# Kernel tuning notes

Measured on AMD Instinct MI355X. Metric: run time of the kernel, lower is better.

## Reference

```python
import jax, jax.numpy as jnp
import numpy as np


def _round_ste(v):
    # straight-through rounding (typical LinearQuantize autograd STE)
    return v + jax.lax.stop_gradient(jnp.round(v) - v)


def setup_inputs() -> dict:
    key = jax.random.key(0)
    k1, k2, k3 = jax.random.split(key, 3)
    tokens, d_in, d_out = 8192, 2048, 2048
    x = jax.random.uniform(k1, (tokens, d_in), dtype=jnp.float32)  # non-negative acts
    weight = jax.random.normal(k2, (d_out, d_in), dtype=jnp.float32) * 0.02
    bias = jax.random.normal(k3, (d_out,), dtype=jnp.float32) * 0.02
    return {"x": x, "weight": weight, "bias": bias, "weight_bit": 8}


def reference(x, weight, bias, weight_bit):
    n = 2 ** weight_bit
    # stats computed on detached data (x.data/w.data in torch)
    wd = jax.lax.stop_gradient(weight)
    w_min = wd.min(axis=1)                      # [out]
    w_max = wd.max(axis=1)                      # [out]
    x_max = jax.lax.stop_gradient(x).max()
    scale_x = (n - 1) / jnp.clip(x_max, 1e-8)
    # activation quantization: round(scale_x * x - 0)
    q_x = _round_ste(scale_x * x)               # [T, in]
    # per-channel asymmetric weight quant (quantize_int)
    scale_w = (n - 1) / jnp.clip(w_max - w_min, 1e-8)   # [out]
    zp_w = scale_w * w_min                      # [out]
    q_w = _round_ste(scale_w[:, None] * weight - zp_w[:, None])  # [out, in]
    # bias quantized with combined scale, then clamped
    q_b = jnp.clip(_round_ste(bias * scale_w * scale_x), -n - 1, n)  # [out]
    # fake-int GEMM + zero-point correction + rescale
    mult = jnp.einsum('ti,oi->to', q_x, q_w) + q_b      # [T, out]
    res = mult + zp_w * q_x.sum(-1, keepdims=True)
    return res / scale_x / scale_w
```

## Files before the change

kernel.cpp:

```cpp
#include <hip/hip_runtime.h>
#include <stdint.h>

typedef __attribute__((ext_vector_type(4))) int i32x4;
typedef __attribute__((ext_vector_type(4))) float f32x4;

__device__ inline float wave_max(float v){ for(int o=32;o;o>>=1) v=fmaxf(v,__shfl_xor(v,o)); return v; }
__device__ inline float wave_min(float v){ for(int o=32;o;o>>=1) v=fminf(v,__shfl_xor(v,o)); return v; }
__device__ inline int   wave_sum(int v){ for(int o=32;o;o>>=1) v+=__shfl_xor(v,o); return v; }

__device__ inline void gload16(const void* g, void* l){
  __builtin_amdgcn_global_load_lds((const __attribute__((address_space(1))) char*)g,
                                   (__attribute__((address_space(3))) char*)l, 16, 0, 0);
}

__global__ void k_xmax_partial(const float* __restrict__ x, long long n4,
                               float* __restrict__ partials){
  long long i = (long long)blockIdx.x*blockDim.x + threadIdx.x;
  long long stride = (long long)gridDim.x*blockDim.x;
  const float4* x4 = (const float4*)x;
  float m = 0.f;
  for(; i < n4; i += stride){
    float4 v = x4[i];
    m = fmaxf(m, fmaxf(fmaxf(v.x,v.y),fmaxf(v.z,v.w)));
  }
  m = wave_max(m);
  __shared__ float sm[4];
  int lane = threadIdx.x & 63, wid = threadIdx.x >> 6;
  if(lane==0) sm[wid] = m;
  __syncthreads();
  if(threadIdx.x==0)
    partials[blockIdx.x] = fmaxf(fmaxf(sm[0],sm[1]),fmaxf(sm[2],sm[3]));
}

__global__ void k_wstat(const float* __restrict__ w,
                        const int* __restrict__ wbit,
                        float* __restrict__ scale_w, float* __restrict__ zp_w,
                        float* __restrict__ winv,
                        int* __restrict__ cint, char* __restrict__ qw, int din){
  int row = blockIdx.x, tid = threadIdx.x;
  int lane = tid & 63, wid = tid >> 6;
  const float4* wr4 = (const float4*)(w + (long long)row*din);
  float4 a = wr4[tid*2], b = wr4[tid*2+1];
  float v[8] = {a.x,a.y,a.z,a.w,b.x,b.y,b.z,b.w};
  float mn = v[0], mx = v[0];
  for(int j=1;j<8;j++){ mn=fminf(mn,v[j]); mx=fmaxf(mx,v[j]); }
  float wmn = wave_min(mn), wmx = wave_max(mx);
  __shared__ float smn[4], smx[4];
  __shared__ float s_sw, s_zp;
  if(lane==0){ smn[wid]=wmn; smx[wid]=wmx; }
  __syncthreads();
  if(tid==0){
    float fmn = fminf(fminf(smn[0],smn[1]),fminf(smn[2],smn[3]));
    float fmx = fmaxf(fmaxf(smx[0],smx[1]),fmaxf(smx[2],smx[3]));
    int n = 1 << *wbit;
    float nm1 = (float)(n-1);
    float rngc = fmaxf(__fsub_rn(fmx, fmn), 1e-8f);
    float sw = __fdiv_rn(nm1, rngc);
    float zp = __fmul_rn(sw, fmn);
    s_sw = sw; s_zp = zp;
    scale_w[row] = sw; zp_w[row] = zp;
    winv[row] = __fdiv_rn(rngc, nm1);
  }
  __syncthreads();
  float sw = s_sw, zp = s_zp;
  int qsum = 0; uint32_t lo = 0, hi = 0;
  for(int j=0;j<8;j++){
    int q = (int)rintf(__fsub_rn(__fmul_rn(sw, v[j]), zp));
    qsum += q;
    uint32_t u = (uint32_t)((q - 128) & 0xff);
    if(j<4) lo |= u << (8*j); else hi |= u << (8*(j-4));
  }
  uint32_t* qrow = (uint32_t*)(qw + (long long)row*din);
  qrow[tid*2] = lo; qrow[tid*2+1] = hi;
  int wsum = wave_sum(qsum);
  __shared__ int ssum[4];
  if(lane==0) ssum[wid] = wsum;
  __syncthreads();
  if(tid==0){
    int Sb = ssum[0]+ssum[1]+ssum[2]+ssum[3];
    cint[row] = 128*Sb - 128*128*din;
  }
}

__global__ void k_xquant(const float* __restrict__ x, const int* __restrict__ wbit,
                         const float* __restrict__ partials, int nPart,
                         char* __restrict__ qx, int* __restrict__ Sa, int din){
  int row = blockIdx.x, tid = threadIdx.x;
  int lane = tid & 63, wid = tid >> 6;
  float mm = 0.f;
  for(int i=tid;i<nPart;i+=256) mm = fmaxf(mm, partials[i]);
  mm = wave_max(mm);
  __shared__ float sm[4];
  if(lane==0) sm[wid] = mm;
  __syncthreads();
  const float xmax = fmaxf(fmaxf(sm[0],sm[1]),fmaxf(sm[2],sm[3]));
  int n = 1 << *wbit;
  float nm1 = (float)(n-1);
  float sx = __fdiv_rn(nm1, fmaxf(xmax, 1e-8f));
  const float4* xr4 = (const float4*)(x + (long long)row*din);
  float4 a = xr4[tid*2], b = xr4[tid*2+1];
  float v[8] = {a.x,a.y,a.z,a.w,b.x,b.y,b.z,b.w};
  int qsum = 0; uint32_t lo = 0, hi = 0;
  for(int j=0;j<8;j++){
    int q = (int)rintf(__fmul_rn(sx, v[j]));
    qsum += q;
    uint32_t u = (uint32_t)((q - 128) & 0xff);
    if(j<4) lo |= u << (8*j); else hi |= u << (8*(j-4));
  }
  uint32_t* qrow = (uint32_t*)(qx + (long long)row*din);
  qrow[tid*2] = lo; qrow[tid*2+1] = hi;
  int wsum = wave_sum(qsum);
  __shared__ int ssum[4];
  if(lane==0) ssum[wid] = wsum;
  __syncthreads();
  if(tid==0) Sa[row] = ssum[0]+ssum[1]+ssum[2]+ssum[3];
}

__global__ __launch_bounds__(512, 2) void k_gemm(
    const char* __restrict__ qx, const char* __restrict__ qw,
    const int* __restrict__ Sa, const int* __restrict__ cint,
    const float* __restrict__ scale_w, const float* __restrict__ winv,
    const float* __restrict__ zp_w, const float* __restrict__ bias,
    const int* __restrict__ wbit, const float* __restrict__ partials, int nPart,
    float* __restrict__ out, int T, int dout, int din){
  extern __shared__ char lds[];
  const int tid = threadIdx.x, lane = tid & 63, wid = tid >> 6;
  const int wr = wid >> 2, wc = wid & 3;
  const int nt = din / 128;

  const int bid = blockIdx.x;
  const int nTN = dout >> 8, nTM = T >> 8;
  int tileM, tileN;
  if(nTM == 32 && nTN == 8){
    const int rect = bid & 7, loc = bid >> 3;
    tileM = (rect >> 1)*8 + (loc & 7);
    tileN = (rect & 1)*4 + (loc >> 3);
  } else {
    tileN = bid % nTN; tileM = bid / nTN;
  }

  const int i0 = tid, i1 = tid + 512;
  const int r0 = i0 >> 2, r1 = i1 >> 2;
  const int sc0 = ((i0 & 3) ^ ((r0 >> 1) & 3)) * 16;
  const int sc1 = ((i1 & 3) ^ ((r1 >> 1) & 3)) * 16;
  const char* aS0 = qx + ((long long)tileM*256 + r0)*din + sc0;
  const char* aS1 = qx + ((long long)tileM*256 + r1)*din + sc1;
  const char* bS0 = qw + ((long long)tileN*256 + r0)*din + sc0;
  const char* bS1 = qw + ((long long)tileN*256 + r1)*din + sc1;
  const int d0 = i0*16, d1 = i1*16;

  const int physo = (((lane >> 4) ^ ((lane >> 1) & 3)) * 16);
  const int arowL = wr*128 + (lane & 15);
  const int browL = wc*64  + (lane & 15);

  i32x4 acc[8][4] = {};
  i32x4 af[4], bf[4];

#define STAGE_A(KS, KOFF, NB) do{ \
    gload16(aS0 + (KOFF) + (KS)*64, (NB) + (KS)*16384 + d0); \
    gload16(aS1 + (KOFF) + (KS)*64, (NB) + (KS)*16384 + d1); }while(0)
#define STAGE_B(KS, KOFF, NB) do{ \
    gload16(bS0 + (KOFF) + (KS)*64, (NB) + 32768 + (KS)*16384 + d0); \
    gload16(bS1 + (KOFF) + (KS)*64, (NB) + 32768 + (KS)*16384 + d1); }while(0)

  STAGE_A(0, 0, lds); STAGE_B(0, 0, lds);
  STAGE_A(1, 0, lds); STAGE_B(1, 0, lds);
  asm volatile("s_waitcnt vmcnt(4)" ::: "memory");
  __builtin_amdgcn_s_barrier();

  for(int t = 0; t < nt; ++t){
    char* Ab = lds + (t & 1)*65536;
    char* Bb = Ab + 32768;
    char* NB = lds + ((t & 1)^1)*65536;
    const bool ld = (t + 1 < nt);
    const int koff = (t + 1)*128;

#define PH(MH, KS, DO_B, STAGE_STMT, VM_STMT) do{ \
    if(DO_B){ _Pragma("unroll") \
      for(int ni=0;ni<4;++ni) bf[ni] = *(const i32x4*)(Bb + (KS)*16384 + (browL + ni*16)*64 + physo); } \
    _Pragma("unroll") \
    for(int mi=0;mi<4;++mi) af[mi] = *(const i32x4*)(Ab + (KS)*16384 + (arowL + (MH)*64 + mi*16)*64 + physo); \
    STAGE_STMT; \
    __builtin_amdgcn_s_barrier(); \
    __builtin_amdgcn_s_setprio(1); \
    _Pragma("unroll") \
    for(int mi=0;mi<4;++mi){ _Pragma("unroll") \
      for(int ni=0;ni<4;++ni) \
        acc[(MH)*4+mi][ni] = __builtin_amdgcn_mfma_i32_16x16x64_i8(af[mi], bf[ni], acc[(MH)*4+mi][ni], 0,0,0); } \
    __builtin_amdgcn_s_setprio(0); \
    VM_STMT; \
    __builtin_amdgcn_s_barrier(); }while(0)

    PH(0, 0, true,  if(ld) STAGE_A(0, koff, NB), );
    PH(1, 0, false, if(ld) STAGE_B(0, koff, NB),
       if(ld){ asm volatile("s_waitcnt vmcnt(4)" ::: "memory"); }
       else  { asm volatile("s_waitcnt vmcnt(0)" ::: "memory"); });
    PH(0, 1, true,  if(ld) STAGE_A(1, koff, NB), );
    PH(1, 1, false, if(ld) STAGE_B(1, koff, NB),
       if(ld){ asm volatile("s_waitcnt vmcnt(4)" ::: "memory"); });
#undef PH
  }

  __syncthreads();
  {
    float mm = 0.f;
    for(int i = tid; i < nPart; i += 512) mm = fmaxf(mm, partials[i]);
    mm = wave_max(mm);
    if(lane==0) ((float*)lds)[wid] = mm;
  }
  __syncthreads();
  float xmax = 0.f;
  #pragma unroll
  for(int i=0;i<8;i++) xmax = fmaxf(xmax, ((float*)lds)[i]);

  const int n = 1 << *wbit;
  const float nm1 = (float)(n-1);
  const float xmaxc = fmaxf(xmax, 1e-8f);
  const float sx = __fdiv_rn(nm1, xmaxc);
  const float inv_sx = __fdiv_rn(xmaxc, nm1);
  const int colL = tileN*256 + wc*64 + (lane & 15);
  const int rowL = tileM*256 + wr*128 + ((lane >> 4) * 4);
  float invc[4], zp4[4]; int ci4[4];
  #pragma unroll
  for(int ni=0; ni<4; ++ni){
    int o = colL + ni*16;
    float sw = scale_w[o];
    float qbf = rintf(__fmul_rn(__fmul_rn(bias[o], sw), sx));
    qbf = fminf(fmaxf(qbf, -(float)(n+1)), (float)n);
    ci4[ni] = cint[o] + (int)qbf;
    invc[ni] = __fmul_rn(winv[o], inv_sx);
    zp4[ni]  = zp_w[o];
  }

  float* ebuf = (float*)lds;
  const int lwr  = wr*16 + ((lane >> 4) * 4);
  const int lcol = wc*64 + (lane & 15);
  #pragma unroll
  for(int mi=0; mi<8; ++mi){
    int rb = rowL + mi*16;
    int sav[4];
    #pragma unroll
    for(int r=0; r<4; ++r) sav[r] = Sa[rb + r];
    __syncthreads();
    #pragma unroll
    for(int ni=0; ni<4; ++ni){
      #pragma unroll
      for(int r=0; r<4; ++r){
        int iv = acc[mi][ni][r] + 128*sav[r] + ci4[ni];
        float f = (float)iv + zp4[ni]*(float)sav[r];
        int row = lwr + r, col = lcol + ni*16;
        ebuf[row*256 + (col ^ (((row>>2)&3)<<4))] = __fmul_rn(f, invc[ni]);
      }
    }
    __syncthreads();
    #pragma unroll
    for(int p=0; p<4; ++p){
      int idx = tid + p*512;
      int lr = idx >> 6, cc = (idx & 63)*4;
      f32x4 v = *(const f32x4*)&ebuf[lr*256 + (cc ^ (((lr>>2)&3)<<4))];
      int gr = tileM*256 + (lr>>4)*128 + mi*16 + (lr&15);
      __builtin_nontemporal_store(v, (f32x4*)&out[(long long)gr*dout + tileN*256 + cc]);
    }
  }
}

extern "C" void kernel_launch(void* const* d_in, const int* in_sizes, int n_in,
                              void* d_out, int out_size, void* d_ws, size_t ws_size,
                              hipStream_t stream){
  const float* x    = (const float*)d_in[0];
  const float* w    = (const float*)d_in[1];
  const float* bias = (const float*)d_in[2];
  const int*   wbit = (const int*)d_in[3];
  int dout = in_sizes[2];
  int din  = in_sizes[1] / dout;
  int T    = in_sizes[0] / din;

  const int NPART = 2048;
  char* ws = (char*)d_ws;
  size_t off = 256;
  float* partials = (float*)(ws + off); off += 4*(size_t)NPART;
  float* scale_w = (float*)(ws + off); off += 4*(size_t)dout;
  float* zp_w    = (float*)(ws + off); off += 4*(size_t)dout;
  float* winv    = (float*)(ws + off); off += 4*(size_t)dout;
  int*   cint    = (int*)(ws + off);   off += 4*(size_t)dout;
  int*   Sa      = (int*)(ws + off);   off += 4*(size_t)T;
  off = (off + 255) & ~(size_t)255;
  char*  qw      = ws + off;           off += (size_t)dout*din;
  char*  qx      = ws + off;           off += (size_t)T*din;

  long long n4 = (long long)T*din/4;
  k_xmax_partial<<<NPART, 256, 0, stream>>>(x, n4, partials);
  k_xquant<<<T, 256, 0, stream>>>(x, wbit, partials, NPART, qx, Sa, din);
  k_wstat<<<dout, 256, 0, stream>>>(w, wbit, scale_w, zp_w, winv, cint, qw, din);
  int nblk = (T/256) * (dout/256);
  k_gemm<<<nblk, 512, 131072, stream>>>(qx, qw, Sa, cint, scale_w, winv, zp_w, bias,
                                        wbit, partials, NPART, (float*)d_out, T, dout, din);
}
```

Before: 81.94 us.

## Pre-tile quantized operands into MFMA fragment layout and load directly to registers

```diff
diff --git a/kernel.cpp b/kernel.cpp
--- a/kernel.cpp
+++ b/kernel.cpp
@@ -7,11 +7,6 @@
 __device__ inline float wave_max(float v){ for(int o=32;o;o>>=1) v=fmaxf(v,__shfl_xor(v,o)); return v; }
 __device__ inline float wave_min(float v){ for(int o=32;o;o>>=1) v=fminf(v,__shfl_xor(v,o)); return v; }
 __device__ inline int   wave_sum(int v){ for(int o=32;o;o>>=1) v+=__shfl_xor(v,o); return v; }
-
-__device__ inline void gload16(const void* g, void* l){
-  __builtin_amdgcn_global_load_lds((const __attribute__((address_space(1))) char*)g,
-                                   (__attribute__((address_space(3))) char*)l, 16, 0, 0);
-}
 
 __global__ void k_xmax_partial(const float* __restrict__ x, long long n4,
                                float* __restrict__ partials){
@@ -30,6 +25,11 @@
   __syncthreads();
   if(threadIdx.x==0)
     partials[blockIdx.x] = fmaxf(fmaxf(sm[0],sm[1]),fmaxf(sm[2],sm[3]));
+}
+
+__device__ inline size_t qoff(int row, int k0, int din){
+  return ((size_t)(row>>4)*(din>>6) + (k0>>6))*1024
+       + (size_t)(((k0&63)>>4)*256 + (row&15)*16 + (k0&15));
 }
 
 __global__ void k_wstat(const float* __restrict__ w,
@@ -70,8 +70,8 @@
     uint32_t u = (uint32_t)((q - 128) & 0xff);
     if(j<4) lo |= u << (8*j); else hi |= u << (8*(j-4));
   }
-  uint32_t* qrow = (uint32_t*)(qw + (long long)row*din);
-  qrow[tid*2] = lo; qrow[tid*2+1] = hi;
+  uint32_t* p = (uint32_t*)(qw + qoff(row, tid*8, din));
+  p[0] = lo; p[1] = hi;
   int wsum = wave_sum(qsum);
   __shared__ int ssum[4];
   if(lane==0) ssum[wid] = wsum;
@@ -107,8 +107,8 @@
     uint32_t u = (uint32_t)((q - 128) & 0xff);
     if(j<4) lo |= u << (8*j); else hi |= u << (8*(j-4));
   }
-  uint32_t* qrow = (uint32_t*)(qx + (long long)row*din);
-  qrow[tid*2] = lo; qrow[tid*2+1] = hi;
+  uint32_t* p = (uint32_t*)(qx + qoff(row, tid*8, din));
+  p[0] = lo; p[1] = hi;
   int wsum = wave_sum(qsum);
   __shared__ int ssum[4];
   if(lane==0) ssum[wid] = wsum;
@@ -123,10 +123,10 @@
     const float* __restrict__ zp_w, const float* __restrict__ bias,
     const int* __restrict__ wbit, const float* __restrict__ partials, int nPart,
     float* __restrict__ out, int T, int dout, int din){
-  extern __shared__ char lds[];
+  __shared__ float ebuf[32*256];
   const int tid = threadIdx.x, lane = tid & 63, wid = tid >> 6;
   const int wr = wid >> 2, wc = wid & 3;
-  const int nt = din / 128;
+  const int nkb = din >> 6;
 
   const int bid = blockIdx.x;
   const int nTN = dout >> 8, nTM = T >> 8;
@@ -139,79 +139,47 @@
     tileN = bid % nTN; tileM = bid / nTN;
   }
 
-  const int i0 = tid, i1 = tid + 512;
-  const int r0 = i0 >> 2, r1 = i1 >> 2;
-  const int sc0 = ((i0 & 3) ^ ((r0 >> 1) & 3)) * 16;
-  const int sc1 = ((i1 & 3) ^ ((r1 >> 1) & 3)) * 16;
-  const char* aS0 = qx + ((long long)tileM*256 + r0)*din + sc0;
-  const char* aS1 = qx + ((long long)tileM*256 + r1)*din + sc1;
-  const char* bS0 = qw + ((long long)tileN*256 + r0)*din + sc0;
-  const char* bS1 = qw + ((long long)tileN*256 + r1)*din + sc1;
-  const int d0 = i0*16, d1 = i1*16;
-
-  const int physo = (((lane >> 4) ^ ((lane >> 1) & 3)) * 16);
-  const int arowL = wr*128 + (lane & 15);
-  const int browL = wc*64  + (lane & 15);
+  const char* aB0 = qx + ((size_t)(tileM*16 + wr*8)*nkb)*1024 + (size_t)lane*16;
+  const char* bB0 = qw + ((size_t)(tileN*16 + wc*4)*nkb)*1024 + (size_t)lane*16;
 
   i32x4 acc[8][4] = {};
-  i32x4 af[4], bf[4];
-
-#define STAGE_A(KS, KOFF, NB) do{ \
-    gload16(aS0 + (KOFF) + (KS)*64, (NB) + (KS)*16384 + d0); \
-    gload16(aS1 + (KOFF) + (KS)*64, (NB) + (KS)*16384 + d1); }while(0)
-#define STAGE_B(KS, KOFF, NB) do{ \
-    gload16(bS0 + (KOFF) + (KS)*64, (NB) + 32768 + (KS)*16384 + d0); \
-    gload16(bS1 + (KOFF) + (KS)*64, (NB) + 32768 + (KS)*16384 + d1); }while(0)
-
-  STAGE_A(0, 0, lds); STAGE_B(0, 0, lds);
-  STAGE_A(1, 0, lds); STAGE_B(1, 0, lds);
-  asm volatile("s_waitcnt vmcnt(4)" ::: "memory");
-  __builtin_amdgcn_s_barrier();
-
-  for(int t = 0; t < nt; ++t){
-    char* Ab = lds + (t & 1)*65536;
-    char* Bb = Ab + 32768;
-    char* NB = lds + ((t & 1)^1)*65536;
-    const bool ld = (t + 1 < nt);
-    const int koff = (t + 1)*128;
-
-#define PH(MH, KS, DO_B, STAGE_STMT, VM_STMT) do{ \
-    if(DO_B){ _Pragma("unroll") \
-      for(int ni=0;ni<4;++ni) bf[ni] = *(const i32x4*)(Bb + (KS)*16384 + (browL + ni*16)*64 + physo); } \
+  i32x4 aX[8], bX[4], aY[8], bY[4];
+
+#define LD(AF, BF, KT) do{ \
     _Pragma("unroll") \
-    for(int mi=0;mi<4;++mi) af[mi] = *(const i32x4*)(Ab + (KS)*16384 + (arowL + (MH)*64 + mi*16)*64 + physo); \
-    STAGE_STMT; \
-    __builtin_amdgcn_s_barrier(); \
+    for(int mi=0;mi<8;++mi) AF[mi] = *(const i32x4*)(aB0 + ((size_t)mi*nkb + (KT))*1024); \
+    _Pragma("unroll") \
+    for(int ni=0;ni<4;++ni) BF[ni] = *(const i32x4*)(bB0 + ((size_t)ni*nkb + (KT))*1024); }while(0)
+#define FM(AF, BF) do{ \
     __builtin_amdgcn_s_setprio(1); \
     _Pragma("unroll") \
-    for(int mi=0;mi<4;++mi){ _Pragma("unroll") \
+    for(int mi=0;mi<8;++mi){ _Pragma("unroll") \
       for(int ni=0;ni<4;++ni) \
-        acc[(MH)*4+mi][ni] = __builtin_amdgcn_mfma_i32_16x16x64_i8(af[mi], bf[ni], acc[(MH)*4+mi][ni], 0,0,0); } \
-    __builtin_amdgcn_s_setprio(0); \
-    VM_STMT; \
-    __builtin_amdgcn_s_barrier(); }while(0)
-
-    PH(0, 0, true,  if(ld) STAGE_A(0, koff, NB), );
-    PH(1, 0, false, if(ld) STAGE_B(0, koff, NB),
-       if(ld){ asm volatile("s_waitcnt vmcnt(4)" ::: "memory"); }
-       else  { asm volatile("s_waitcnt vmcnt(0)" ::: "memory"); });
-    PH(0, 1, true,  if(ld) STAGE_A(1, koff, NB), );
-    PH(1, 1, false, if(ld) STAGE_B(1, koff, NB),
-       if(ld){ asm volatile("s_waitcnt vmcnt(4)" ::: "memory"); });
-#undef PH
-  }
-
-  __syncthreads();
-  {
-    float mm = 0.f;
-    for(int i = tid; i < nPart; i += 512) mm = fmaxf(mm, partials[i]);
-    mm = wave_max(mm);
-    if(lane==0) ((float*)lds)[wid] = mm;
-  }
-  __syncthreads();
+        acc[mi][ni] = __builtin_amdgcn_mfma_i32_16x16x64_i8(AF[mi], BF[ni], acc[mi][ni], 0,0,0); } \
+    __builtin_amdgcn_s_setprio(0); }while(0)
+
+  LD(aX, bX, 0);
+  for(int kt = 0; kt < nkb; kt += 2){
+    if(kt + 1 < nkb) LD(aY, bY, kt+1);
+    FM(aX, bX);
+    if(kt + 2 < nkb) LD(aX, bX, kt+2);
+    FM(aY, bY);
+  }
+#undef LD
+#undef FM
+
+#define EBAR do{ asm volatile("s_waitcnt lgkmcnt(0)" ::: "memory"); \
+                 __builtin_amdgcn_s_barrier(); }while(0)
+
+  float mm = 0.f;
+  for(int i = tid; i < nPart; i += 512) mm = fmaxf(mm, partials[i]);
+  mm = wave_max(mm);
+  if(lane==0) ebuf[wid] = mm;
+  EBAR;
   float xmax = 0.f;
   #pragma unroll
-  for(int i=0;i<8;i++) xmax = fmaxf(xmax, ((float*)lds)[i]);
+  for(int i=0;i<8;i++) xmax = fmaxf(xmax, ebuf[i]);
+  EBAR;
 
   const int n = 1 << *wbit;
   const float nm1 = (float)(n-1);
@@ -232,7 +200,6 @@
     zp4[ni]  = zp_w[o];
   }
 
-  float* ebuf = (float*)lds;
   const int lwr  = wr*16 + ((lane >> 4) * 4);
   const int lcol = wc*64 + (lane & 15);
   #pragma unroll
@@ -241,7 +208,7 @@
     int sav[4];
     #pragma unroll
     for(int r=0; r<4; ++r) sav[r] = Sa[rb + r];
-    __syncthreads();
+    EBAR;
     #pragma unroll
     for(int ni=0; ni<4; ++ni){
       #pragma unroll
@@ -252,7 +219,7 @@
         ebuf[row*256 + (col ^ (((row>>2)&3)<<4))] = __fmul_rn(f, invc[ni]);
       }
     }
-    __syncthreads();
+    EBAR;
     #pragma unroll
     for(int p=0; p<4; ++p){
       int idx = tid + p*512;
@@ -262,6 +229,7 @@
       __builtin_nontemporal_store(v, (f32x4*)&out[(long long)gr*dout + tileN*256 + cc]);
     }
   }
+#undef EBAR
 }
 
 extern "C" void kernel_launch(void* const* d_in, const int* in_sizes, int n_in,
@@ -293,6 +261,6 @@
   k_xquant<<<T, 256, 0, stream>>>(x, wbit, partials, NPART, qx, Sa, din);
   k_wstat<<<dout, 256, 0, stream>>>(w, wbit, scale_w, zp_w, winv, cint, qw, din);
   int nblk = (T/256) * (dout/256);
-  k_gemm<<<nblk, 512, 131072, stream>>>(qx, qw, Sa, cint, scale_w, winv, zp_w, bias,
-                                        wbit, partials, NPART, (float*)d_out, T, dout, din);
-}
+  k_gemm<<<nblk, 512, 0, stream>>>(qx, qw, Sa, cint, scale_w, winv, zp_w, bias,
+                                   wbit, partials, NPART, (float*)d_out, T, dout, din);
+}
```

Result: slower. 139.4 us (+70.1%).
